# Kernel optimization log

Measured on AMD Instinct MI355X. Metric: run time of the kernel, lower is better.

## Reference

```python
import jax, jax.numpy as jnp
import numpy as np

N_NODES = 10000
N_EDGES = 160000
IN_FEAT = 1024
H_FEAT = 1024
NUM_CLASSES = 64


def setup_inputs() -> dict:
    key = jax.random.key(0)
    ks = jax.random.split(key, 8)
    h = jax.random.normal(ks[0], (N_NODES, IN_FEAT), dtype=jnp.float32)
    src = jax.random.randint(ks[1], (N_EDGES,), 0, N_NODES, dtype=jnp.int32)
    dst = jax.random.randint(ks[2], (N_EDGES,), 0, N_NODES, dtype=jnp.int32)
    # Xavier-ish scaled weights (DGL uses xavier_uniform for GraphConv)
    W1 = jax.random.normal(ks[3], (IN_FEAT, H_FEAT), dtype=jnp.float32) * (1.0 / np.sqrt(IN_FEAT))
    b1 = jnp.zeros((H_FEAT,), dtype=jnp.float32)
    W2 = jax.random.normal(ks[4], (H_FEAT, H_FEAT), dtype=jnp.float32) * (1.0 / np.sqrt(H_FEAT))
    b2 = jnp.zeros((H_FEAT,), dtype=jnp.float32)
    W3 = jax.random.normal(ks[5], (H_FEAT, NUM_CLASSES), dtype=jnp.float32) * (1.0 / np.sqrt(H_FEAT))
    b3 = jnp.zeros((NUM_CLASSES,), dtype=jnp.float32)
    return {"h": h, "src": src, "dst": dst,
            "W1": W1, "b1": b1, "W2": W2, "b2": b2, "W3": W3, "b3": b3}


def _graph_conv(src, dst, norm_src, norm_dst, x, W, b):
    """DGL GraphConv with norm='both':
    out = D_dst^{-1/2} * sum_{(u,v) in E} (D_src^{-1/2} * x)_u  @ W + b
    """
    xs = x * norm_src[:, None]                     # [N, d] scaled source feats
    msg = xs[src]                                  # [E, d] gather
    agg = jax.ops.segment_sum(msg, dst, num_segments=N_NODES)  # [N, d] scatter-add
    agg = agg * norm_dst[:, None]
    return agg @ W + b


def reference(h, src, dst, W1, b1, W2, b2, W3, b3):
    ones = jnp.ones((N_EDGES,), dtype=jnp.float32)
    deg_out = jax.ops.segment_sum(ones, src, num_segments=N_NODES)  # out-degree of src
    deg_in = jax.ops.segment_sum(ones, dst, num_segments=N_NODES)   # in-degree of dst
    norm_src = jnp.clip(deg_out, 1.0, None) ** -0.5
    norm_dst = jnp.clip(deg_in, 1.0, None) ** -0.5

    x = _graph_conv(src, dst, norm_src, norm_dst, h, W1, b1)
    x = jax.nn.relu(x)
    x = _graph_conv(src, dst, norm_src, norm_dst, x, W2, b2)
    x = jax.nn.relu(x)
    x = _graph_conv(src, dst, norm_src, norm_dst, x, W3, b3)
    return x
```

## Files before the change

kernel.cpp:

```cpp
#include <hip/hip_runtime.h>

constexpr int NN   = 10000;
constexpr int NE   = 160000;
constexpr int F    = 1024;
constexpr int C3   = 64;
constexpr int MPAD = 10112;

typedef __attribute__((ext_vector_type(8))) short short8;
typedef __attribute__((ext_vector_type(8))) unsigned short ushort8v;
typedef __attribute__((ext_vector_type(4))) float floatx4;

__device__ __forceinline__ unsigned short f2bf(float f) {
    union { float f; unsigned u; } v; v.f = f;
    unsigned r = v.u + 0x7fff + ((v.u >> 16) & 1);
    return (unsigned short)(r >> 16);
}
__device__ __forceinline__ float bf2f(unsigned short u) {
    union { unsigned u; float f; } v; v.u = ((unsigned)u) << 16;
    return v.f;
}

__device__ __forceinline__ void gl_lds16(const void* g, void* l) {
    __builtin_amdgcn_global_load_lds(
        (const __attribute__((address_space(1))) unsigned int*)g,
        (__attribute__((address_space(3))) unsigned int*)l, 16, 0, 0);
}


__global__ __launch_bounds__(256) void k_degree(const int* __restrict__ src,
                                                const int* __restrict__ dst,
                                                int* __restrict__ deg_out,
                                                int* __restrict__ deg_in) {
    int e = blockIdx.x * 256 + threadIdx.x;
    if (e < NE) {
        atomicAdd(&deg_out[src[e]], 1);
        atomicAdd(&deg_in[dst[e]], 1);
    }
}

__global__ __launch_bounds__(256) void k_norm(const int* __restrict__ deg_out,
                                              const int* __restrict__ deg_in,
                                              float* __restrict__ norm_src,
                                              float* __restrict__ norm_dst) {
    int v = blockIdx.x * 256 + threadIdx.x;
    if (v < MPAD) {
        norm_src[v] = rsqrtf(fmaxf((float)deg_out[v], 1.0f));
        norm_dst[v] = rsqrtf(fmaxf((float)deg_in[v], 1.0f));
    }
}

__global__ __launch_bounds__(1024) void k_scan(const int* __restrict__ deg_in,
                                               int* __restrict__ row_ptr,
                                               int* __restrict__ cursor) {
    constexpr int CH = 10;
    __shared__ int sums[1024];
    const int tid = threadIdx.x;
    int local[CH];
    int tsum = 0;
#pragma unroll
    for (int j = 0; j < CH; ++j) {
        int idx = tid * CH + j;
        int v = (idx < NN) ? deg_in[idx] : 0;
        local[j] = v;
        tsum += v;
    }
    sums[tid] = tsum;
    __syncthreads();
    for (int off = 1; off < 1024; off <<= 1) {
        int v = (tid >= off) ? sums[tid - off] : 0;
        __syncthreads();
        sums[tid] += v;
        __syncthreads();
    }
    int run = sums[tid] - tsum;
#pragma unroll
    for (int j = 0; j < CH; ++j) {
        int idx = tid * CH + j;
        if (idx < NN) {
            row_ptr[idx] = run;
            cursor[idx]  = run;
        }
        run += local[j];
    }
    if (tid == 1023) row_ptr[NN] = sums[1023];
}

__global__ __launch_bounds__(256) void k_bucket(const int* __restrict__ src,
                                                const int* __restrict__ dst,
                                                int* __restrict__ cursor,
                                                int* __restrict__ csr_src) {
    int e = blockIdx.x * 256 + threadIdx.x;
    if (e < NE) {
        int slot = atomicAdd(&cursor[dst[e]], 1);
        csr_src[slot] = src[e];
    }
}


__global__ __launch_bounds__(256) void k_wconv(const float* __restrict__ W,
                                               unsigned short* __restrict__ Wt,
                                               int N) {
    __shared__ float tile[32][33];
    const int n0 = blockIdx.x * 32, k0 = blockIdx.y * 32;
    const int tx = threadIdx.x & 31, ty = threadIdx.x >> 5;
#pragma unroll
    for (int i = 0; i < 32; i += 8)
        tile[ty + i][tx] = W[(size_t)(k0 + ty + i) * N + n0 + tx];
    __syncthreads();
#pragma unroll
    for (int i = 0; i < 32; i += 8)
        Wt[(size_t)(n0 + ty + i) * F + k0 + tx] = f2bf(tile[tx][ty + i]);
}


__global__ __launch_bounds__(256) void k_hcvt(const float* __restrict__ h,
                                              const float* __restrict__ norm_src,
                                              unsigned short* __restrict__ hb) {
    int idx = blockIdx.x * 256 + threadIdx.x;
    int v = idx >> 7, f8 = (idx & 127) * 8;
    float ns = norm_src[v];
    const float4 a = *(const float4*)(h + (size_t)v * F + f8);
    const float4 b = *(const float4*)(h + (size_t)v * F + f8 + 4);
    ushort8v o;
    o[0] = f2bf(ns * a.x); o[1] = f2bf(ns * a.y);
    o[2] = f2bf(ns * a.z); o[3] = f2bf(ns * a.w);
    o[4] = f2bf(ns * b.x); o[5] = f2bf(ns * b.y);
    o[6] = f2bf(ns * b.z); o[7] = f2bf(ns * b.w);
    *(ushort8v*)(hb + (size_t)v * F + f8) = o;
}

__global__ __launch_bounds__(256) void k_aggb(const unsigned short* __restrict__ xb,
                                              const int* __restrict__ row_ptr,
                                              const int* __restrict__ csr_src,
                                              unsigned short* __restrict__ aggb) {
    const int c = blockIdx.x & 7;
    const int g = blockIdx.x >> 3;
    const int v = g * 16 + (threadIdx.x >> 4);
    const int f8 = c * 128 + (threadIdx.x & 15) * 8;
    const int lo = row_ptr[v], hi = row_ptr[v + 1];
    float acc[8] = {0.f, 0.f, 0.f, 0.f, 0.f, 0.f, 0.f, 0.f};
    int i = lo;
    for (; i + 2 <= hi; i += 2) {
        int s0 = csr_src[i], s1 = csr_src[i + 1];
        ushort8v x0 = *(const ushort8v*)(xb + (size_t)s0 * F + f8);
        ushort8v x1 = *(const ushort8v*)(xb + (size_t)s1 * F + f8);
#pragma unroll
        for (int j = 0; j < 8; ++j) acc[j] += bf2f(x0[j]);
#pragma unroll
        for (int j = 0; j < 8; ++j) acc[j] += bf2f(x1[j]);
    }
    if (i < hi) {
        int s = csr_src[i];
        ushort8v xv = *(const ushort8v*)(xb + (size_t)s * F + f8);
#pragma unroll
        for (int j = 0; j < 8; ++j) acc[j] += bf2f(xv[j]);
    }
    ushort8v o;
#pragma unroll
    for (int j = 0; j < 8; ++j) o[j] = f2bf(acc[j]);
    *(ushort8v*)(aggb + (size_t)v * F + f8) = o;
}

__global__ __launch_bounds__(256) void k_agg64(const float* __restrict__ z,
                                               const int* __restrict__ row_ptr,
                                               const int* __restrict__ csr_src,
                                               const float* __restrict__ norm_dst,
                                               const float* __restrict__ b3,
                                               float* __restrict__ out) {
    const int v = blockIdx.x * 16 + (threadIdx.x >> 4);
    if (v >= NN) return;
    const int f4 = (threadIdx.x & 15) * 4;
    const int lo = row_ptr[v], hi = row_ptr[v + 1];
    float4 acc = {0.f, 0.f, 0.f, 0.f};
    for (int i = lo; i < hi; ++i) {
        int s = csr_src[i];
        float4 zv = *(const float4*)(z + (size_t)s * C3 + f4);
        acc.x += zv.x; acc.y += zv.y; acc.z += zv.z; acc.w += zv.w;
    }
    float nd = norm_dst[v];
    float4 bv = *(const float4*)(b3 + f4);
    float4 o;
    o.x = acc.x * nd + bv.x; o.y = acc.y * nd + bv.y;
    o.z = acc.z * nd + bv.z; o.w = acc.w * nd + bv.w;
    *(float4*)(out + (size_t)v * C3 + f4) = o;
}

__global__ __launch_bounds__(256) void k_gemm_bf16(
        const unsigned short* __restrict__ A,
        const unsigned short* __restrict__ Bt,
        const float* __restrict__ bias,
        const float* __restrict__ rs1,
        const float* __restrict__ rs2,
        unsigned short* __restrict__ Cb) {
    const int bid = blockIdx.x;
    const int xcd = bid & 7, idx = bid >> 3;
    const int g   = xcd * 79 + idx;
    const int m0  = (g >> 3) * 128, n0 = (g & 7) * 128;

    __shared__ short As[2][128 * 32];
    __shared__ short Bs[2][128 * 32];
    const int t = threadIdx.x, lane = t & 63, wid = t >> 6;
    const int wm0 = (wid & 1) * 64, wn0 = (wid >> 1) * 64;
    const int lr = lane & 15, q = lane >> 4;

    int srow[2], soff[2];
#pragma unroll
    for (int j = 0; j < 2; ++j) {
        int i = wid + j * 4;
        int r = i * 16 + (lane >> 2);
        srow[j] = r;
        soff[j] = (((lane & 3) ^ ((r >> 1) & 3)) * 8);
    }
    const unsigned short* aSrc0 = A  + (size_t)(m0 + srow[0]) * F + soff[0];
    const unsigned short* aSrc1 = A  + (size_t)(m0 + srow[1]) * F + soff[1];
    const unsigned short* bSrc0 = Bt + (size_t)(n0 + srow[0]) * F + soff[0];
    const unsigned short* bSrc1 = Bt + (size_t)(n0 + srow[1]) * F + soff[1];

    const short* ap[4];
    const short* bp[4];
#pragma unroll
    for (int mb = 0; mb < 4; ++mb) {
        int m = wm0 + mb * 16 + lr;
        ap[mb] = &As[0][m * 32 + (q ^ ((m >> 1) & 3)) * 8];
        int n = wn0 + mb * 16 + lr;
        bp[mb] = &Bs[0][n * 32 + (q ^ ((n >> 1) & 3)) * 8];
    }

    floatx4 acc[4][4] = {};

    gl_lds16(aSrc0, &As[0][(wid)     * 512]);
    gl_lds16(aSrc1, &As[0][(wid + 4) * 512]);
    gl_lds16(bSrc0, &Bs[0][(wid)     * 512]);
    gl_lds16(bSrc1, &Bs[0][(wid + 4) * 512]);

    for (int kt = 0; kt < F / 32; ++kt) {
        const int buf = kt & 1;
        __syncthreads();
        if (kt + 1 < F / 32) {
            int k0 = (kt + 1) * 32;
            gl_lds16(aSrc0 + k0, &As[buf ^ 1][(wid)     * 512]);
            gl_lds16(aSrc1 + k0, &As[buf ^ 1][(wid + 4) * 512]);
            gl_lds16(bSrc0 + k0, &Bs[buf ^ 1][(wid)     * 512]);
            gl_lds16(bSrc1 + k0, &Bs[buf ^ 1][(wid + 4) * 512]);
        }
        const int bo = buf * (128 * 32);
        short8 af[4], bf[4];
#pragma unroll
        for (int mb = 0; mb < 4; ++mb) af[mb] = *(const short8*)(ap[mb] + bo);
#pragma unroll
        for (int nb = 0; nb < 4; ++nb) bf[nb] = *(const short8*)(bp[nb] + bo);
#pragma unroll
        for (int mb = 0; mb < 4; ++mb)
#pragma unroll
            for (int nb = 0; nb < 4; ++nb)
                acc[mb][nb] = __builtin_amdgcn_mfma_f32_16x16x32_bf16(
                    af[mb], bf[nb], acc[mb][nb], 0, 0, 0);
    }

    float s1[4][4], s2[4][4];
#pragma unroll
    for (int mb = 0; mb < 4; ++mb)
#pragma unroll
        for (int r = 0; r < 4; ++r) {
            int row = m0 + wm0 + mb * 16 + q * 4 + r;
            s1[mb][r] = rs1[row];
            s2[mb][r] = rs2[row];
        }
#pragma unroll
    for (int nb = 0; nb < 4; ++nb) {
        int col = n0 + wn0 + nb * 16 + lr;
        float bv = bias[col];
#pragma unroll
        for (int mb = 0; mb < 4; ++mb)
#pragma unroll
            for (int r = 0; r < 4; ++r) {
                int row = m0 + wm0 + mb * 16 + q * 4 + r;
                float v = fmaxf(acc[mb][nb][r] * s1[mb][r] + bv, 0.f) * s2[mb][r];
                Cb[(size_t)row * F + col] = f2bf(v);
            }
    }
}

__global__ __launch_bounds__(256) void k_gemm3(
        const unsigned short* __restrict__ A,
        const unsigned short* __restrict__ Bt,
        float* __restrict__ Z) {
    __shared__ short As3[2][64 * 32];
    __shared__ short Bs3[2][64 * 32];
    const int t = threadIdx.x, lane = t & 63, wid = t >> 6;
    const int m0 = blockIdx.x * 64;
    const int lr = lane & 15, q = lane >> 4;

    const int r = wid * 16 + (lane >> 2);
    const int soff = (((lane & 3) ^ ((r >> 1) & 3)) * 8);
    const unsigned short* aSrc = A  + (size_t)(m0 + r) * F + soff;
    const unsigned short* bSrc = Bt + (size_t)r * F + soff;

    const short* ap;
    {
        int m = wid * 16 + lr;
        ap = &As3[0][m * 32 + (q ^ ((m >> 1) & 3)) * 8];
    }
    const short* bp[4];
#pragma unroll
    for (int nb = 0; nb < 4; ++nb) {
        int n = nb * 16 + lr;
        bp[nb] = &Bs3[0][n * 32 + (q ^ ((n >> 1) & 3)) * 8];
    }

    floatx4 acc[4] = {};

    gl_lds16(aSrc, &As3[0][wid * 512]);
    gl_lds16(bSrc, &Bs3[0][wid * 512]);

    for (int kt = 0; kt < F / 32; ++kt) {
        const int buf = kt & 1;
        __syncthreads();
        if (kt + 1 < F / 32) {
            int k0 = (kt + 1) * 32;
            gl_lds16(aSrc + k0, &As3[buf ^ 1][wid * 512]);
            gl_lds16(bSrc + k0, &Bs3[buf ^ 1][wid * 512]);
        }
        const int bo = buf * (64 * 32);
        short8 af = *(const short8*)(ap + bo);
        short8 bf[4];
#pragma unroll
        for (int nb = 0; nb < 4; ++nb) bf[nb] = *(const short8*)(bp[nb] + bo);
#pragma unroll
        for (int nb = 0; nb < 4; ++nb)
            acc[nb] = __builtin_amdgcn_mfma_f32_16x16x32_bf16(af, bf[nb], acc[nb], 0, 0, 0);
    }

#pragma unroll
    for (int nb = 0; nb < 4; ++nb) {
        int col = nb * 16 + lr;
#pragma unroll
        for (int ri = 0; ri < 4; ++ri) {
            int row = m0 + wid * 16 + q * 4 + ri;
            Z[(size_t)row * C3 + col] = acc[nb][ri];
        }
    }
}


extern "C" void kernel_launch(void* const* d_in, const int* in_sizes, int n_in,
                              void* d_out, int out_size, void* d_ws, size_t ws_size,
                              hipStream_t stream) {
    const float* h   = (const float*)d_in[0];
    const int*   src = (const int*)d_in[1];
    const int*   dst = (const int*)d_in[2];
    const float* W1  = (const float*)d_in[3];
    const float* b1  = (const float*)d_in[4];
    const float* W2  = (const float*)d_in[5];
    const float* b2  = (const float*)d_in[6];
    const float* W3  = (const float*)d_in[7];
    const float* b3  = (const float*)d_in[8];
    float* out = (float*)d_out;

    char* ws = (char*)d_ws;
    int*   deg_out  = (int*)ws;                       ws += MPAD * 4;
    int*   deg_in   = (int*)ws;                       ws += MPAD * 4;
    float* norm_src = (float*)ws;                     ws += MPAD * 4;
    float* norm_dst = (float*)ws;                     ws += MPAD * 4;
    int*   row_ptr  = (int*)ws;                       ws += (NN + 1) * 4;
    int*   cursor   = (int*)ws;                       ws += NN * 4;
    int*   csr_src  = (int*)ws;                       ws += NE * 4;
    ws = (char*)(((size_t)ws + 255) & ~(size_t)255);
    unsigned short* hb   = (unsigned short*)ws;       ws += (size_t)MPAD * F * 2;
    unsigned short* aggb = (unsigned short*)ws;       ws += (size_t)MPAD * F * 2;
    unsigned short* xb   = (unsigned short*)ws;       ws += (size_t)MPAD * F * 2;
    unsigned short* Wt1  = (unsigned short*)ws;       ws += (size_t)F * F * 2;
    unsigned short* Wt2  = (unsigned short*)ws;       ws += (size_t)F * F * 2;
    unsigned short* Wt3  = (unsigned short*)ws;       ws += (size_t)C3 * F * 2;
    float* z3       = (float*)ws;

    hipMemsetAsync(deg_out, 0, 2 * MPAD * sizeof(int), stream);
    k_degree<<<(NE + 255) / 256, 256, 0, stream>>>(src, dst, deg_out, deg_in);
    k_norm<<<(MPAD + 255) / 256, 256, 0, stream>>>(deg_out, deg_in, norm_src, norm_dst);
    k_scan<<<1, 1024, 0, stream>>>(deg_in, row_ptr, cursor);
    k_bucket<<<(NE + 255) / 256, 256, 0, stream>>>(src, dst, cursor, csr_src);
    k_wconv<<<dim3(F / 32, F / 32), 256, 0, stream>>>(W1, Wt1, F);
    k_wconv<<<dim3(F / 32, F / 32), 256, 0, stream>>>(W2, Wt2, F);
    k_wconv<<<dim3(C3 / 32, F / 32), 256, 0, stream>>>(W3, Wt3, C3);
    k_hcvt<<<NN * 128 / 256, 256, 0, stream>>>(h, norm_src, hb);

    k_aggb<<<(NN / 16) * 8, 256, 0, stream>>>(hb, row_ptr, csr_src, aggb);
    k_gemm_bf16<<<(MPAD / 128) * (F / 128), 256, 0, stream>>>(aggb, Wt1, b1, norm_dst, norm_src, xb);

    k_aggb<<<(NN / 16) * 8, 256, 0, stream>>>(xb, row_ptr, csr_src, aggb);
    k_gemm_bf16<<<(MPAD / 128) * (F / 128), 256, 0, stream>>>(aggb, Wt2, b2, norm_dst, norm_src, xb);

    k_gemm3<<<MPAD / 64, 256, 0, stream>>>(xb, Wt3, z3);
    k_agg64<<<(NN + 15) / 16, 256, 0, stream>>>(z3, row_ptr, csr_src, norm_dst, b3, out);
}
```

Before: 302.2 us.

## Use 128x64 tiles with triple-buffered LDS pipeline in bf16 GEMM

The main bf16 GEMM moves from 128x128 tiles with double buffering to 128x64 tiles with a three-stage LDS ring. It issues loads two k-steps ahead and waits with explicit vmcnt plus a raw barrier instead of __syncthreads. The XCD-aware block remapping is dropped in favour of a plain 2D grid. This doubles the block count (79 to 158 per column band) to fill more CUs and hides more global-load latency, at the cost of lower per-block operand reuse and less L2 locality from the removed XCD swizzle.

```diff
diff --git a/kernel.cpp b/kernel.cpp
--- a/kernel.cpp
+++ b/kernel.cpp
@@ -192,67 +192,73 @@
         const float* __restrict__ rs1,
         const float* __restrict__ rs2,
         unsigned short* __restrict__ Cb) {
-    const int bid = blockIdx.x;
-    const int xcd = bid & 7, idx = bid >> 3;
-    const int g   = xcd * 79 + idx;
-    const int m0  = (g >> 3) * 128, n0 = (g & 7) * 128;
-
-    __shared__ short As[2][128 * 32];
-    __shared__ short Bs[2][128 * 32];
+    constexpr int NT = F / 32;
+    __shared__ short As[3][128 * 32];
+    __shared__ short Bs[3][64 * 32];
     const int t = threadIdx.x, lane = t & 63, wid = t >> 6;
-    const int wm0 = (wid & 1) * 64, wn0 = (wid >> 1) * 64;
+    const int m0 = blockIdx.x * 128, n0 = blockIdx.y * 64;
+    const int wm0 = (wid & 1) * 64, wn0 = (wid >> 1) * 32;
     const int lr = lane & 15, q = lane >> 4;
 
-    int srow[2], soff[2];
-#pragma unroll
-    for (int j = 0; j < 2; ++j) {
-        int i = wid + j * 4;
-        int r = i * 16 + (lane >> 2);
-        srow[j] = r;
-        soff[j] = (((lane & 3) ^ ((r >> 1) & 3)) * 8);
-    }
-    const unsigned short* aSrc0 = A  + (size_t)(m0 + srow[0]) * F + soff[0];
-    const unsigned short* aSrc1 = A  + (size_t)(m0 + srow[1]) * F + soff[1];
-    const unsigned short* bSrc0 = Bt + (size_t)(n0 + srow[0]) * F + soff[0];
-    const unsigned short* bSrc1 = Bt + (size_t)(n0 + srow[1]) * F + soff[1];
+    const int rA0 = wid * 16 + (lane >> 2);
+    const int rA1 = (wid + 4) * 16 + (lane >> 2);
+    const int rB  = wid * 16 + (lane >> 2);
+    const int sA0 = (((lane & 3) ^ ((rA0 >> 1) & 3)) * 8);
+    const int sA1 = (((lane & 3) ^ ((rA1 >> 1) & 3)) * 8);
+    const int sB  = (((lane & 3) ^ ((rB  >> 1) & 3)) * 8);
+    const unsigned short* aSrc0 = A  + (size_t)(m0 + rA0) * F + sA0;
+    const unsigned short* aSrc1 = A  + (size_t)(m0 + rA1) * F + sA1;
+    const unsigned short* bSrc  = Bt + (size_t)(n0 + rB)  * F + sB;
+    short* aDst0 = &As[0][(wid)     * 512];
+    short* aDst1 = &As[0][(wid + 4) * 512];
+    short* bDst  = &Bs[0][(wid)     * 512];
 
     const short* ap[4];
-    const short* bp[4];
+    const short* bp[2];
 #pragma unroll
     for (int mb = 0; mb < 4; ++mb) {
         int m = wm0 + mb * 16 + lr;
         ap[mb] = &As[0][m * 32 + (q ^ ((m >> 1) & 3)) * 8];
-        int n = wn0 + mb * 16 + lr;
-        bp[mb] = &Bs[0][n * 32 + (q ^ ((n >> 1) & 3)) * 8];
-    }
-
-    floatx4 acc[4][4] = {};
-
-    gl_lds16(aSrc0, &As[0][(wid)     * 512]);
-    gl_lds16(aSrc1, &As[0][(wid + 4) * 512]);
-    gl_lds16(bSrc0, &Bs[0][(wid)     * 512]);
-    gl_lds16(bSrc1, &Bs[0][(wid + 4) * 512]);
-
-    for (int kt = 0; kt < F / 32; ++kt) {
-        const int buf = kt & 1;
-        __syncthreads();
-        if (kt + 1 < F / 32) {
-            int k0 = (kt + 1) * 32;
-            gl_lds16(aSrc0 + k0, &As[buf ^ 1][(wid)     * 512]);
-            gl_lds16(aSrc1 + k0, &As[buf ^ 1][(wid + 4) * 512]);
-            gl_lds16(bSrc0 + k0, &Bs[buf ^ 1][(wid)     * 512]);
-            gl_lds16(bSrc1 + k0, &Bs[buf ^ 1][(wid + 4) * 512]);
-        }
-        const int bo = buf * (128 * 32);
-        short8 af[4], bf[4];
-#pragma unroll
-        for (int mb = 0; mb < 4; ++mb) af[mb] = *(const short8*)(ap[mb] + bo);
-#pragma unroll
-        for (int nb = 0; nb < 4; ++nb) bf[nb] = *(const short8*)(bp[nb] + bo);
+    }
+#pragma unroll
+    for (int nb = 0; nb < 2; ++nb) {
+        int n = wn0 + nb * 16 + lr;
+        bp[nb] = &Bs[0][n * 32 + (q ^ ((n >> 1) & 3)) * 8];
+    }
+
+    floatx4 acc[4][2] = {};
+
+    gl_lds16(aSrc0,      aDst0);
+    gl_lds16(aSrc1,      aDst1);
+    gl_lds16(bSrc,       bDst);
+    gl_lds16(aSrc0 + 32, aDst0 + 4096);
+    gl_lds16(aSrc1 + 32, aDst1 + 4096);
+    gl_lds16(bSrc  + 32, bDst  + 2048);
+
+    for (int kt = 0; kt < NT; ++kt) {
+        if (kt < NT - 1) {
+            asm volatile("s_waitcnt vmcnt(3)\n\ts_barrier" ::: "memory");
+        } else {
+            asm volatile("s_waitcnt vmcnt(0)\n\ts_barrier" ::: "memory");
+        }
+        if (kt + 2 < NT) {
+            const int pb = (kt + 2) % 3;
+            const int k0 = (kt + 2) * 32;
+            gl_lds16(aSrc0 + k0, aDst0 + pb * 4096);
+            gl_lds16(aSrc1 + k0, aDst1 + pb * 4096);
+            gl_lds16(bSrc  + k0, bDst  + pb * 2048);
+        }
+        const int ba = (kt % 3) * 4096;
+        const int bb = (kt % 3) * 2048;
+        short8 af[4], bf[2];
+#pragma unroll
+        for (int mb = 0; mb < 4; ++mb) af[mb] = *(const short8*)(ap[mb] + ba);
+#pragma unroll
+        for (int nb = 0; nb < 2; ++nb) bf[nb] = *(const short8*)(bp[nb] + bb);
 #pragma unroll
         for (int mb = 0; mb < 4; ++mb)
 #pragma unroll
-            for (int nb = 0; nb < 4; ++nb)
+            for (int nb = 0; nb < 2; ++nb)
                 acc[mb][nb] = __builtin_amdgcn_mfma_f32_16x16x32_bf16(
                     af[mb], bf[nb], acc[mb][nb], 0, 0, 0);
     }
@@ -267,7 +273,7 @@
             s2[mb][r] = rs2[row];
         }
 #pragma unroll
-    for (int nb = 0; nb < 4; ++nb) {
+    for (int nb = 0; nb < 2; ++nb) {
         int col = n0 + wn0 + nb * 16 + lr;
         float bv = bias[col];
 #pragma unroll
@@ -385,10 +391,10 @@
     k_hcvt<<<NN * 128 / 256, 256, 0, stream>>>(h, norm_src, hb);
 
     k_aggb<<<(NN / 16) * 8, 256, 0, stream>>>(hb, row_ptr, csr_src, aggb);
-    k_gemm_bf16<<<(MPAD / 128) * (F / 128), 256, 0, stream>>>(aggb, Wt1, b1, norm_dst, norm_src, xb);
+    k_gemm_bf16<<<dim3(MPAD / 128, F / 64), 256, 0, stream>>>(aggb, Wt1, b1, norm_dst, norm_src, xb);
 
     k_aggb<<<(NN / 16) * 8, 256, 0, stream>>>(xb, row_ptr, csr_src, aggb);
-    k_gemm_bf16<<<(MPAD / 128) * (F / 128), 256, 0, stream>>>(aggb, Wt2, b2, norm_dst, norm_src, xb);
+    k_gemm_bf16<<<dim3(MPAD / 128, F / 64), 256, 0, stream>>>(aggb, Wt2, b2, norm_dst, norm_src, xb);
 
     k_gemm3<<<MPAD / 64, 256, 0, stream>>>(xb, Wt3, z3);
     k_agg64<<<(NN + 15) / 16, 256, 0, stream>>>(z3, row_ptr, csr_src, norm_dst, b3, out);
```

Measured after the change: 341.5 us. 13.0% more time.
